# Kernel optimization log

Measured on AMD Instinct MI355X. Metric: run time of the kernel, lower is better.

## Reference

```python
import jax, jax.numpy as jnp
import numpy as np

EMB = 1024
HEADS = 16
HEAD_DIM = EMB // HEADS
DFF = 4 * EMB
EPS = 1e-5


def setup_inputs() -> dict:
    key = jax.random.key(0)
    ks = jax.random.split(key, 16)
    s = 0.02
    return {
        "x": jax.random.normal(ks[0], (4, 2048, EMB), dtype=jnp.float32),
        "Wq_w": jax.random.normal(ks[1], (EMB, EMB), jnp.float32) * s,
        "Wq_b": jnp.zeros((EMB,), jnp.float32),
        "Wk_w": jax.random.normal(ks[2], (EMB, EMB), jnp.float32) * s,
        "Wk_b": jnp.zeros((EMB,), jnp.float32),
        "Wv_w": jax.random.normal(ks[3], (EMB, EMB), jnp.float32) * s,
        "Wv_b": jnp.zeros((EMB,), jnp.float32),
        "Wo_w": jax.random.normal(ks[4], (EMB, EMB), jnp.float32) * s,
        "Wo_b": jnp.zeros((EMB,), jnp.float32),
        "l1_w": jax.random.normal(ks[5], (DFF, EMB), jnp.float32) * s,
        "l1_b": jnp.zeros((DFF,), jnp.float32),
        "l2_w": jax.random.normal(ks[6], (EMB, DFF), jnp.float32) * s,
        "l2_b": jnp.zeros((EMB,), jnp.float32),
        "n1_scale": jnp.ones((EMB,), jnp.float32),
        "n1_shift": jnp.zeros((EMB,), jnp.float32),
        "n2_scale": jnp.ones((EMB,), jnp.float32),
        "n2_shift": jnp.zeros((EMB,), jnp.float32),
    }


def _layernorm(x, scale, shift):
    # Faithful to the source: mean over last dim, but var over the WHOLE
    # tensor (torch.var with no dim), and divides by var (not std), eps added after.
    mean = jnp.mean(x, axis=-1, keepdims=True)
    var = jnp.var(x)  # scalar, correction=0
    x_norm = (x - mean) / var + EPS
    return x_norm * scale + shift


def _block_forward(x, Wq_w, Wq_b, Wk_w, Wk_b, Wv_w, Wv_b, Wo_w, Wo_b,
                   l1_w, l1_b, l2_w, l2_b, n1_scale, n1_shift, n2_scale, n2_shift):
    B, T, C = x.shape
    shortcut = x
    h = _layernorm(x, n1_scale, n1_shift)

    def proj(w, b):
        y = jnp.einsum('btc,oc->bto', h, w) + b
        return y.reshape(B, T, HEADS, HEAD_DIM).transpose(0, 2, 1, 3)  # bhtd

    q = proj(Wq_w, Wq_b)
    k = proj(Wk_w, Wk_b)
    v = proj(Wv_w, Wv_b)

    scores = jnp.einsum('bhtd,bhsd->bhts', q, k)
    causal = jnp.triu(jnp.ones((T, T), dtype=bool), 1)
    scores = jnp.where(causal, -jnp.inf, scores)
    weights = jax.nn.softmax(scores / jnp.sqrt(jnp.float32(HEAD_DIM)), axis=-1)
    ctx = jnp.einsum('bhts,bhsd->bhtd', weights, v)
    ctx = ctx.transpose(0, 2, 1, 3).reshape(B, T, C)
    attn_out = jnp.einsum('btc,oc->bto', ctx, Wo_w) + Wo_b

    x = attn_out + shortcut
    shortcut = x
    h = _layernorm(x, n2_scale, n2_shift)
    h = jnp.einsum('btc,fc->btf', h, l1_w) + l1_b
    h = jax.nn.gelu(h, approximate=False)
    h = jnp.einsum('btf,cf->btc', h, l2_w) + l2_b
    return h + shortcut


def reference(x, Wq_w, Wq_b, Wk_w, Wk_b, Wv_w, Wv_b, Wo_w, Wo_b,
              l1_w, l1_b, l2_w, l2_b, n1_scale, n1_shift, n2_scale, n2_shift):
    return _block_forward(x, Wq_w, Wq_b, Wk_w, Wk_b, Wv_w, Wv_b, Wo_w, Wo_b,
                          l1_w, l1_b, l2_w, l2_b, n1_scale, n1_shift, n2_scale, n2_shift)
```

## Files before the change

### kernel.cpp

```cpp
#include <hip/hip_runtime.h>
#include <cstdint>

#define EMB   1024
#define HEADS 16
#define HDIM  64
#define DFF   4096
#define TLEN  2048
#define BATCH 4
#define SEQB  8192
#define EPSLN 1e-5f

typedef __attribute__((ext_vector_type(8))) short bf16x8;
typedef __attribute__((ext_vector_type(4))) float f32x4;

#define MFMA16(a, b, c) __builtin_amdgcn_mfma_f32_16x16x32_bf16((a), (b), (c), 0, 0, 0)

__device__ __forceinline__ unsigned short f2bf(float f) {
  unsigned int u = __float_as_uint(f);
  u += 0x7fffu + ((u >> 16) & 1u);
  return (unsigned short)(u >> 16);
}

__device__ __forceinline__ float gelu_f(float x) {
  float x2 = x * x;
  float inner = x * (0.79788456f + 0.035677408f * x2);
  float t = exp2f(2.885390082f * inner);
  return x * t / (t + 1.0f);
}

__global__ __launch_bounds__(256) void cvt_bf16(const float* __restrict__ in,
                                                unsigned short* __restrict__ out, int n4) {
  int i = blockIdx.x * 256 + threadIdx.x;
  if (i >= n4) return;
  float4 v = ((const float4*)in)[i];
  ushort4 o;
  o.x = f2bf(v.x); o.y = f2bf(v.y); o.z = f2bf(v.z); o.w = f2bf(v.w);
  ((ushort4*)out)[i] = o;
}

__global__ __launch_bounds__(256) void pack3(const float* __restrict__ a,
                                             const float* __restrict__ b,
                                             const float* __restrict__ c,
                                             float* __restrict__ o) {
  int i = blockIdx.x * 256 + threadIdx.x;
  o[i] = i < 1024 ? a[i] : (i < 2048 ? b[i - 1024] : c[i - 2048]);
}

__global__ __launch_bounds__(256) void row_reduce(const float* __restrict__ X,
                                                  float* __restrict__ rs,
                                                  float* __restrict__ rq) {
  const int row = blockIdx.x;
  const int tid = threadIdx.x;
  float4 v = ((const float4*)(X + (long)row * EMB))[tid];
  float s = v.x + v.y + v.z + v.w;
  float q = v.x * v.x + v.y * v.y + v.z * v.z + v.w * v.w;
#pragma unroll
  for (int d = 1; d < 64; d <<= 1) { s += __shfl_xor(s, d); q += __shfl_xor(q, d); }
  __shared__ float ss[4], sq[4];
  const int wv = tid >> 6;
  if ((tid & 63) == 0) { ss[wv] = s; sq[wv] = q; }
  __syncthreads();
  if (tid == 0) {
    rs[row] = ss[0] + ss[1] + ss[2] + ss[3];
    rq[row] = sq[0] + sq[1] + sq[2] + sq[3];
  }
}

__global__ __launch_bounds__(256) void finalize_stats(const float* __restrict__ rs,
                                                      const float* __restrict__ rq,
                                                      float* __restrict__ stats) {
  const int tid = threadIdx.x;
  float s = 0.f, q = 0.f;
  for (int i = tid; i < SEQB; i += 256) { s += rs[i]; q += rq[i]; }
#pragma unroll
  for (int d = 1; d < 64; d <<= 1) { s += __shfl_xor(s, d); q += __shfl_xor(q, d); }
  __shared__ float ss[4], sq[4];
  const int wv = tid >> 6;
  if ((tid & 63) == 0) { ss[wv] = s; sq[wv] = q; }
  __syncthreads();
  if (tid == 0) {
    double n = (double)SEQB * (double)EMB;
    double mean = (double)(ss[0] + ss[1] + ss[2] + ss[3]) / n;
    double var = (double)(sq[0] + sq[1] + sq[2] + sq[3]) / n - mean * mean;
    stats[0] = (float)(1.0 / var);
  }
}

__global__ __launch_bounds__(256) void ln_apply(const float* __restrict__ X,
                                                const float* __restrict__ rs,
                                                const float* __restrict__ stats,
                                                const float* __restrict__ scale,
                                                const float* __restrict__ shift,
                                                unsigned short* __restrict__ H) {
  const long i = (long)blockIdx.x * 256 + threadIdx.x;
  const long idx = i * 4;
  const int row = (int)(idx >> 10);
  const int c = (int)(idx & 1023);
  const float mean = rs[row] * (1.0f / EMB);
  const float iv = stats[0];
  float4 x = ((const float4*)X)[i];
  float4 sc = *(const float4*)(scale + c);
  float4 sh = *(const float4*)(shift + c);
  ushort4 o;
  o.x = f2bf(((x.x - mean) * iv + EPSLN) * sc.x + sh.x);
  o.y = f2bf(((x.y - mean) * iv + EPSLN) * sc.y + sh.y);
  o.z = f2bf(((x.z - mean) * iv + EPSLN) * sc.z + sh.z);
  o.w = f2bf(((x.w - mean) * iv + EPSLN) * sc.w + sh.w);
  ((ushort4*)H)[i] = o;
}

template <int EPI>
__global__ __launch_bounds__(256) void gemm_bt(const unsigned short* __restrict__ A,
                                               const unsigned short* __restrict__ W,
                                               const float* __restrict__ bias,
                                               const float* __restrict__ resid,
                                               void* __restrict__ Cout,
                                               unsigned short* __restrict__ kout,
                                               unsigned short* __restrict__ vout,
                                               int M, int N, int K) {
  __shared__ unsigned short sA[128 * 64];
  __shared__ unsigned short sB[128 * 64];
  const int tid = threadIdx.x;
  const int lane = tid & 63;
  const int wave = tid >> 6;
  const int wm = (wave >> 1) * 64, wn = (wave & 1) * 64;
  const int col = lane & 15, quad = lane >> 4;
  const int cx = (col & 7) * 8;

  const int gx = (int)gridDim.x, gy = (int)gridDim.y;
  const int nwg = gx * gy;
  int bid = (int)blockIdx.y * gx + (int)blockIdx.x;
  if ((nwg & 7) == 0) bid = (bid & 7) * (nwg >> 3) + (bid >> 3);
  const int bx = bid % gx;
  const int by = bid / gx;
  const long bm = (long)by * 128, bn = (long)bx * 128;

  f32x4 acc[4][4];
#pragma unroll
  for (int i = 0; i < 4; ++i)
#pragma unroll
    for (int j = 0; j < 4; ++j) acc[i][j] = (f32x4){0.f, 0.f, 0.f, 0.f};

  const int r0 = tid >> 3;
  const int kg = (tid & 7) * 8;
  const int rx = (r0 & 7) * 8;
  const int kgx = kg ^ rx;

  for (int k0 = 0; k0 < K; k0 += 64) {
#pragma unroll
    for (int it = 0; it < 4; ++it) {
      const int r = it * 32 + r0;
      const unsigned short* ga = A + (bm + r) * K + k0 + kgx;
      const unsigned short* gb = W + (bn + r) * K + k0 + kgx;
      __builtin_amdgcn_global_load_lds((const __attribute__((address_space(1))) void*)ga,
                                       (__attribute__((address_space(3))) void*)&sA[r * 64 + kg],
                                       16, 0, 0);
      __builtin_amdgcn_global_load_lds((const __attribute__((address_space(1))) void*)gb,
                                       (__attribute__((address_space(3))) void*)&sB[r * 64 + kg],
                                       16, 0, 0);
    }
    __syncthreads();
#pragma unroll
    for (int ks = 0; ks < 2; ++ks) {
      const int off = (ks * 32 + quad * 8) ^ cx;
      bf16x8 af[4], bfr[4];
#pragma unroll
      for (int mt = 0; mt < 4; ++mt)
        af[mt] = *(const bf16x8*)&sA[(wm + mt * 16 + col) * 64 + off];
#pragma unroll
      for (int nt = 0; nt < 4; ++nt)
        bfr[nt] = *(const bf16x8*)&sB[(wn + nt * 16 + col) * 64 + off];
#pragma unroll
      for (int mt = 0; mt < 4; ++mt)
#pragma unroll
        for (int nt = 0; nt < 4; ++nt) acc[mt][nt] = MFMA16(af[mt], bfr[nt], acc[mt][nt]);
    }
    __syncthreads();
  }

#pragma unroll
  for (int mt = 0; mt < 4; ++mt) {
    const long row0 = bm + wm + mt * 16 + quad * 4;
#pragma unroll
    for (int nt = 0; nt < 4; ++nt) {
      const long c = bn + wn + nt * 16 + col;
      const float bv = bias[c];
      if (EPI == 4) {
        const int seg = (int)(bn >> 10);
        if (seg == 2) {
          ushort4 o;
#pragma unroll
          for (int r = 0; r < 4; ++r) o[r] = f2bf(acc[mt][nt][r] + bv);
          const long bidx = row0 >> 11;
          const long t0 = row0 & 2047;
          *(ushort4*)(vout + (((bidx * 1024 + (c & 1023)) << 11) + t0)) = o;
        } else {
          unsigned short* dst = seg == 0 ? (unsigned short*)Cout : kout;
#pragma unroll
          for (int r = 0; r < 4; ++r)
            dst[(row0 + r) * 1024 + (c & 1023)] = f2bf(acc[mt][nt][r] + bv);
        }
      } else {
#pragma unroll
        for (int r = 0; r < 4; ++r) {
          const long row = row0 + r;
          float v = acc[mt][nt][r] + bv;
          if (EPI == 0) {
            ((unsigned short*)Cout)[row * N + c] = f2bf(v);
          } else if (EPI == 1) {
            ((float*)Cout)[row * N + c] = v + resid[row * N + c];
          } else {
            ((unsigned short*)Cout)[row * N + c] = f2bf(gelu_f(v));
          }
        }
      }
    }
  }
}

#define PSTR 136
__global__ __launch_bounds__(512, 4) void attn10(const unsigned short* __restrict__ Qb,
                                                 const unsigned short* __restrict__ Kb,
                                                 const unsigned short* __restrict__ vT,
                                                 unsigned short* __restrict__ Ctx) {
  __shared__ unsigned short sK[128 * 64];
  __shared__ unsigned short sV[64 * 128];
  __shared__ unsigned short sP[8][16 * PSTR];
  const int bh = blockIdx.x;
  const int pair = blockIdx.y;
  const int b = bh >> 4, h = bh & 15;
  const int tid = threadIdx.x, lane = tid & 63, w = tid >> 6;
  const int col = lane & 15, quad = lane >> 4;
  const int cx = (col & 7) * 8;
  const long bbase = (long)b * TLEN;
  const long hoff = (long)h * HDIM;
  const unsigned short* vbase = vT + (((long)b * 16 + h) * HDIM << 11);
  const float sc2 = 0.125f * 1.44269504088896340736f;

  const int krow = tid >> 3;
  const int kcol = ((tid & 7) * 8) ^ ((krow & 7) * 8);
  const int vrow = tid >> 4;
  const int vcol = ((tid & 15) * 8) ^ ((vrow & 7) * 8);

  for (int phase = 0; phase < 2; ++phase) {
    const int qt = phase == 0 ? (15 - pair) : pair;

    bf16x8 qf[2];
    {
      const long t = (long)qt * 128 + w * 16 + col;
      const unsigned short* qp = Qb + (bbase + t) * EMB + hoff;
#pragma unroll
      for (int ks = 0; ks < 2; ++ks) qf[ks] = *(const bf16x8*)(qp + ks * 32 + quad * 8);
    }

    float li[4] = {0.f, 0.f, 0.f, 0.f};
    f32x4 o[4];
#pragma unroll
    for (int dt = 0; dt < 4; ++dt) o[dt] = (f32x4){0.f, 0.f, 0.f, 0.f};

    for (int kv = 0; kv <= qt; ++kv) {
      __syncthreads();
#pragma unroll
      for (int it = 0; it < 2; ++it) {
        const unsigned short* gk = Kb + (bbase + (long)kv * 128 + it * 64 + krow) * EMB + hoff + kcol;
        __builtin_amdgcn_global_load_lds((const __attribute__((address_space(1))) void*)gk,
                                         (__attribute__((address_space(3))) void*)&sK[it * 4096 + tid * 8],
                                         16, 0, 0);
        const unsigned short* gv = vbase + ((long)(it * 32 + vrow) << 11) + kv * 128 + vcol;
        __builtin_amdgcn_global_load_lds((const __attribute__((address_space(1))) void*)gv,
                                         (__attribute__((address_space(3))) void*)&sV[it * 4096 + tid * 8],
                                         16, 0, 0);
      }
      __syncthreads();

      f32x4 sa[8];
#pragma unroll
      for (int nt = 0; nt < 8; ++nt) sa[nt] = (f32x4){0.f, 0.f, 0.f, 0.f};
#pragma unroll
      for (int ks = 0; ks < 2; ++ks) {
        const int off = (ks * 32 + quad * 8) ^ cx;
#pragma unroll
        for (int nt = 0; nt < 8; ++nt) {
          bf16x8 kf = *(const bf16x8*)&sK[(nt * 16 + col) * 64 + off];
          sa[nt] = MFMA16(qf[ks], kf, sa[nt]);
        }
      }

      if (kv == qt) {
#pragma unroll
        for (int nt = 0; nt < 8; ++nt)
#pragma unroll
          for (int r = 0; r < 4; ++r) {
            const int trel = w * 16 + quad * 4 + r;
            const int srel = nt * 16 + col;
            if (srel > trel) sa[nt][r] = -INFINITY;
          }
      }

#pragma unroll
      for (int nt = 0; nt < 8; ++nt)
#pragma unroll
        for (int r = 0; r < 4; ++r) {
          const float p = exp2f(sa[nt][r] * sc2);
          li[r] += p;
          sP[w][(quad * 4 + r) * PSTR + nt * 16 + col] = f2bf(p);
        }

#pragma unroll
      for (int ks = 0; ks < 4; ++ks) {
        bf16x8 pa = *(const bf16x8*)&sP[w][col * PSTR + ks * 32 + quad * 8];
        const int voff = (ks * 32 + quad * 8) ^ cx;
#pragma unroll
        for (int dt = 0; dt < 4; ++dt) {
          bf16x8 vf = *(const bf16x8*)&sV[(dt * 16 + col) * 128 + voff];
          o[dt] = MFMA16(pa, vf, o[dt]);
        }
      }
    }

#pragma unroll
    for (int d = 1; d < 16; d <<= 1)
#pragma unroll
      for (int r = 0; r < 4; ++r) li[r] += __shfl_xor(li[r], d);

#pragma unroll
    for (int r = 0; r < 4; ++r) {
      const float inv = 1.0f / li[r];
#pragma unroll
      for (int dt = 0; dt < 4; ++dt)
        sP[w][(quad * 4 + r) * 72 + dt * 16 + col] = f2bf(o[dt][r] * inv);
    }
#pragma unroll
    for (int p = 0; p < 2; ++p) {
      const int rr = (lane >> 3) + p * 8;
      bf16x8 vrow = *(const bf16x8*)&sP[w][rr * 72 + (lane & 7) * 8];
      const long t = (long)qt * 128 + w * 16 + rr;
      *(bf16x8*)(Ctx + (bbase + t) * EMB + hoff + (lane & 7) * 8) = vrow;
    }
  }
}

extern "C" void kernel_launch(void* const* d_in, const int* in_sizes, int n_in,
                              void* d_out, int out_size, void* d_ws, size_t ws_size,
                              hipStream_t stream) {
  const float* x    = (const float*)d_in[0];
  const float* Wq_w = (const float*)d_in[1];
  const float* Wq_b = (const float*)d_in[2];
  const float* Wk_w = (const float*)d_in[3];
  const float* Wk_b = (const float*)d_in[4];
  const float* Wv_w = (const float*)d_in[5];
  const float* Wv_b = (const float*)d_in[6];
  const float* Wo_w = (const float*)d_in[7];
  const float* Wo_b = (const float*)d_in[8];
  const float* l1_w = (const float*)d_in[9];
  const float* l1_b = (const float*)d_in[10];
  const float* l2_w = (const float*)d_in[11];
  const float* l2_b = (const float*)d_in[12];
  const float* n1s  = (const float*)d_in[13];
  const float* n1h  = (const float*)d_in[14];
  const float* n2s  = (const float*)d_in[15];
  const float* n2h  = (const float*)d_in[16];

  char* ws = (char*)d_ws;
  const size_t MB = (size_t)1 << 20;
  unsigned short* wqkv = (unsigned short*)(ws + 0 * MB);
  unsigned short* wo = (unsigned short*)(ws + 6 * MB);
  unsigned short* l1 = (unsigned short*)(ws + 8 * MB);
  unsigned short* l2 = (unsigned short*)(ws + 16 * MB);
  unsigned short* hb = (unsigned short*)(ws + 24 * MB);
  unsigned short* qb = (unsigned short*)(ws + 40 * MB);
  unsigned short* kb = (unsigned short*)(ws + 56 * MB);
  unsigned short* vb = (unsigned short*)(ws + 72 * MB);
  unsigned short* cb = (unsigned short*)(ws + 88 * MB);
  unsigned short* gb = qb;
  float* x2 = (float*)(ws + 104 * MB);
  float* rs = (float*)(ws + 136 * MB);
  float* rq = (float*)(ws + 136 * MB + 64 * 1024);
  float* st = (float*)(ws + 136 * MB + 128 * 1024);
  float* bqkv = (float*)(ws + 136 * MB + 192 * 1024);

  cvt_bf16<<<1024, 256, 0, stream>>>(Wq_w, wqkv, EMB * EMB / 4);
  cvt_bf16<<<1024, 256, 0, stream>>>(Wk_w, wqkv + 1024 * 1024, EMB * EMB / 4);
  cvt_bf16<<<1024, 256, 0, stream>>>(Wv_w, wqkv + 2048 * 1024, EMB * EMB / 4);
  cvt_bf16<<<1024, 256, 0, stream>>>(Wo_w, wo, EMB * EMB / 4);
  cvt_bf16<<<4096, 256, 0, stream>>>(l1_w, l1, DFF * EMB / 4);
  cvt_bf16<<<4096, 256, 0, stream>>>(l2_w, l2, EMB * DFF / 4);
  pack3<<<12, 256, 0, stream>>>(Wq_b, Wk_b, Wv_b, bqkv);

  row_reduce<<<SEQB, 256, 0, stream>>>(x, rs, rq);
  finalize_stats<<<1, 256, 0, stream>>>(rs, rq, st);
  ln_apply<<<SEQB, 256, 0, stream>>>(x, rs, st, n1s, n1h, hb);

  dim3 g1(EMB / 128, SEQB / 128);
  gemm_bt<4><<<dim3(3 * EMB / 128, SEQB / 128), 256, 0, stream>>>(
      hb, wqkv, bqkv, nullptr, qb, kb, vb, SEQB, 3 * EMB, EMB);

  attn10<<<dim3(BATCH * HEADS, 8), 512, 0, stream>>>(qb, kb, vb, cb);

  gemm_bt<1><<<g1, 256, 0, stream>>>(cb, wo, Wo_b, x, (void*)x2, nullptr, nullptr, SEQB, EMB, EMB);

  row_reduce<<<SEQB, 256, 0, stream>>>(x2, rs, rq);
  finalize_stats<<<1, 256, 0, stream>>>(rs, rq, st);
  ln_apply<<<SEQB, 256, 0, stream>>>(x2, rs, st, n2s, n2h, hb);

  gemm_bt<2><<<dim3(DFF / 128, SEQB / 128), 256, 0, stream>>>(hb, l1, l1_b, nullptr, gb, nullptr, nullptr, SEQB, DFF, EMB);
  gemm_bt<1><<<g1, 256, 0, stream>>>(gb, l2, l2_b, x2, d_out, nullptr, nullptr, SEQB, EMB, DFF);
}
```

Before: 540.6 us.

## Fuse prep kernels and compute LN2 row stats in out-proj GEMM epilogue

Merges the six weight-conversion launches, the bias packing, the first row-reduction and the zeroing of new stat buffers into one large prep kernel. Adds a GEMM epilogue variant for the attention output projection that adds the residual and accumulates per-row sum and sum-of-squares via shuffles and atomics. This removes the separate row_reduce pass over x2. In exchange it adds atomic traffic and float-ordering nondeterminism in the row statistics.

Measured after the change: 540.7 us. Within noise of the previous version (+0.0%).

```diff
diff --git a/kernel.cpp b/kernel.cpp
--- a/kernel.cpp
+++ b/kernel.cpp
@@ -28,41 +28,55 @@
   return x * t / (t + 1.0f);
 }
 
-__global__ __launch_bounds__(256) void cvt_bf16(const float* __restrict__ in,
-                                                unsigned short* __restrict__ out, int n4) {
-  int i = blockIdx.x * 256 + threadIdx.x;
-  if (i >= n4) return;
-  float4 v = ((const float4*)in)[i];
-  ushort4 o;
-  o.x = f2bf(v.x); o.y = f2bf(v.y); o.z = f2bf(v.z); o.w = f2bf(v.w);
-  ((ushort4*)out)[i] = o;
-}
-
-__global__ __launch_bounds__(256) void pack3(const float* __restrict__ a,
-                                             const float* __restrict__ b,
-                                             const float* __restrict__ c,
-                                             float* __restrict__ o) {
-  int i = blockIdx.x * 256 + threadIdx.x;
-  o[i] = i < 1024 ? a[i] : (i < 2048 ? b[i - 1024] : c[i - 2048]);
-}
-
-__global__ __launch_bounds__(256) void row_reduce(const float* __restrict__ X,
-                                                  float* __restrict__ rs,
-                                                  float* __restrict__ rq) {
-  const int row = blockIdx.x;
+__global__ __launch_bounds__(256) void prep(const float* __restrict__ wq, const float* __restrict__ wk,
+                                            const float* __restrict__ wv, const float* __restrict__ wom,
+                                            const float* __restrict__ l1w, const float* __restrict__ l2w,
+                                            unsigned short* __restrict__ wqkv, unsigned short* __restrict__ wo,
+                                            unsigned short* __restrict__ l1, unsigned short* __restrict__ l2,
+                                            const float* __restrict__ bq, const float* __restrict__ bk,
+                                            const float* __restrict__ bv, float* __restrict__ bqkv,
+                                            const float* __restrict__ X, float* __restrict__ rs,
+                                            float* __restrict__ rq, float* __restrict__ rs2,
+                                            float* __restrict__ rq2) {
+  __shared__ float ss[4], sq[4];
+  const int bid = blockIdx.x;
   const int tid = threadIdx.x;
-  float4 v = ((const float4*)(X + (long)row * EMB))[tid];
-  float s = v.x + v.y + v.z + v.w;
-  float q = v.x * v.x + v.y * v.y + v.z * v.z + v.w * v.w;
-#pragma unroll
-  for (int d = 1; d < 64; d <<= 1) { s += __shfl_xor(s, d); q += __shfl_xor(q, d); }
-  __shared__ float ss[4], sq[4];
-  const int wv = tid >> 6;
-  if ((tid & 63) == 0) { ss[wv] = s; sq[wv] = q; }
-  __syncthreads();
-  if (tid == 0) {
-    rs[row] = ss[0] + ss[1] + ss[2] + ss[3];
-    rq[row] = sq[0] + sq[1] + sq[2] + sq[3];
+  if (bid < 12288) {
+    const float* src;
+    unsigned short* dst;
+    int off;
+    if (bid < 1024)      { src = wq;  dst = wqkv;               off = bid; }
+    else if (bid < 2048) { src = wk;  dst = wqkv + (1 << 20);   off = bid - 1024; }
+    else if (bid < 3072) { src = wv;  dst = wqkv + (2 << 20);   off = bid - 2048; }
+    else if (bid < 4096) { src = wom; dst = wo;                 off = bid - 3072; }
+    else if (bid < 8192) { src = l1w; dst = l1;                 off = bid - 4096; }
+    else                 { src = l2w; dst = l2;                 off = bid - 8192; }
+    const int i = off * 256 + tid;
+    float4 v = ((const float4*)src)[i];
+    ushort4 o;
+    o.x = f2bf(v.x); o.y = f2bf(v.y); o.z = f2bf(v.z); o.w = f2bf(v.w);
+    ((ushort4*)dst)[i] = o;
+  } else if (bid < 20480) {
+    const int row = bid - 12288;
+    float4 v = ((const float4*)(X + (long)row * EMB))[tid];
+    float s = v.x + v.y + v.z + v.w;
+    float q = v.x * v.x + v.y * v.y + v.z * v.z + v.w * v.w;
+#pragma unroll
+    for (int d = 1; d < 64; d <<= 1) { s += __shfl_xor(s, d); q += __shfl_xor(q, d); }
+    const int wv_ = tid >> 6;
+    if ((tid & 63) == 0) { ss[wv_] = s; sq[wv_] = q; }
+    __syncthreads();
+    if (tid == 0) {
+      rs[row] = ss[0] + ss[1] + ss[2] + ss[3];
+      rq[row] = sq[0] + sq[1] + sq[2] + sq[3];
+    }
+  } else if (bid < 20492) {
+    const int i = (bid - 20480) * 256 + tid;
+    bqkv[i] = i < 1024 ? bq[i] : (i < 2048 ? bk[i - 1024] : bv[i - 2048]);
+  } else {
+    const int i = (bid - 20492) * 256 + tid;
+    if (i < 2048) ((float4*)rs2)[i] = (float4){0.f, 0.f, 0.f, 0.f};
+    else          ((float4*)rq2)[i - 2048] = (float4){0.f, 0.f, 0.f, 0.f};
   }
 }
 
@@ -181,36 +195,67 @@
 #pragma unroll
   for (int mt = 0; mt < 4; ++mt) {
     const long row0 = bm + wm + mt * 16 + quad * 4;
-#pragma unroll
-    for (int nt = 0; nt < 4; ++nt) {
-      const long c = bn + wn + nt * 16 + col;
-      const float bv = bias[c];
-      if (EPI == 4) {
-        const int seg = (int)(bn >> 10);
-        if (seg == 2) {
-          ushort4 o;
-#pragma unroll
-          for (int r = 0; r < 4; ++r) o[r] = f2bf(acc[mt][nt][r] + bv);
-          const long bidx = row0 >> 11;
-          const long t0 = row0 & 2047;
-          *(ushort4*)(vout + (((bidx * 1024 + (c & 1023)) << 11) + t0)) = o;
-        } else {
-          unsigned short* dst = seg == 0 ? (unsigned short*)Cout : kout;
-#pragma unroll
-          for (int r = 0; r < 4; ++r)
-            dst[(row0 + r) * 1024 + (c & 1023)] = f2bf(acc[mt][nt][r] + bv);
-        }
-      } else {
+    if (EPI == 3) {
+      float s4[4] = {0.f, 0.f, 0.f, 0.f}, q4[4] = {0.f, 0.f, 0.f, 0.f};
+#pragma unroll
+      for (int nt = 0; nt < 4; ++nt) {
+        const long c = bn + wn + nt * 16 + col;
+        const float bv = bias[c];
 #pragma unroll
         for (int r = 0; r < 4; ++r) {
           const long row = row0 + r;
-          float v = acc[mt][nt][r] + bv;
-          if (EPI == 0) {
-            ((unsigned short*)Cout)[row * N + c] = f2bf(v);
-          } else if (EPI == 1) {
-            ((float*)Cout)[row * N + c] = v + resid[row * N + c];
+          const float v = acc[mt][nt][r] + bv + resid[row * N + c];
+          ((float*)Cout)[row * N + c] = v;
+          s4[r] += v;
+          q4[r] += v * v;
+        }
+      }
+#pragma unroll
+      for (int r = 0; r < 4; ++r)
+#pragma unroll
+        for (int d = 1; d < 16; d <<= 1) {
+          s4[r] += __shfl_xor(s4[r], d);
+          q4[r] += __shfl_xor(q4[r], d);
+        }
+      if (col == 0) {
+#pragma unroll
+        for (int r = 0; r < 4; ++r) {
+          atomicAdd((float*)kout + row0 + r, s4[r]);
+          atomicAdd((float*)vout + row0 + r, q4[r]);
+        }
+      }
+    } else {
+#pragma unroll
+      for (int nt = 0; nt < 4; ++nt) {
+        const long c = bn + wn + nt * 16 + col;
+        const float bv = bias[c];
+        if (EPI == 4) {
+          const int seg = (int)(bn >> 10);
+          if (seg == 2) {
+            ushort4 o;
+#pragma unroll
+            for (int r = 0; r < 4; ++r) o[r] = f2bf(acc[mt][nt][r] + bv);
+            const long bidx = row0 >> 11;
+            const long t0 = row0 & 2047;
+            *(ushort4*)(vout + (((bidx * 1024 + (c & 1023)) << 11) + t0)) = o;
           } else {
-            ((unsigned short*)Cout)[row * N + c] = f2bf(gelu_f(v));
+            unsigned short* dst = seg == 0 ? (unsigned short*)Cout : kout;
+#pragma unroll
+            for (int r = 0; r < 4; ++r)
+              dst[(row0 + r) * 1024 + (c & 1023)] = f2bf(acc[mt][nt][r] + bv);
+          }
+        } else {
+#pragma unroll
+          for (int r = 0; r < 4; ++r) {
+            const long row = row0 + r;
+            float v = acc[mt][nt][r] + bv;
+            if (EPI == 0) {
+              ((unsigned short*)Cout)[row * N + c] = f2bf(v);
+            } else if (EPI == 1) {
+              ((float*)Cout)[row * N + c] = v + resid[row * N + c];
+            } else {
+              ((unsigned short*)Cout)[row * N + c] = f2bf(gelu_f(v));
+            }
           }
         }
       }
@@ -378,16 +423,12 @@
   float* rq = (float*)(ws + 136 * MB + 64 * 1024);
   float* st = (float*)(ws + 136 * MB + 128 * 1024);
   float* bqkv = (float*)(ws + 136 * MB + 192 * 1024);
-
-  cvt_bf16<<<1024, 256, 0, stream>>>(Wq_w, wqkv, EMB * EMB / 4);
-  cvt_bf16<<<1024, 256, 0, stream>>>(Wk_w, wqkv + 1024 * 1024, EMB * EMB / 4);
-  cvt_bf16<<<1024, 256, 0, stream>>>(Wv_w, wqkv + 2048 * 1024, EMB * EMB / 4);
-  cvt_bf16<<<1024, 256, 0, stream>>>(Wo_w, wo, EMB * EMB / 4);
-  cvt_bf16<<<4096, 256, 0, stream>>>(l1_w, l1, DFF * EMB / 4);
-  cvt_bf16<<<4096, 256, 0, stream>>>(l2_w, l2, EMB * DFF / 4);
-  pack3<<<12, 256, 0, stream>>>(Wq_b, Wk_b, Wv_b, bqkv);
-
-  row_reduce<<<SEQB, 256, 0, stream>>>(x, rs, rq);
+  float* rs2 = (float*)(ws + 136 * MB + 256 * 1024);
+  float* rq2 = (float*)(ws + 136 * MB + 320 * 1024);
+
+  prep<<<20508, 256, 0, stream>>>(Wq_w, Wk_w, Wv_w, Wo_w, l1_w, l2_w, wqkv, wo, l1, l2,
+                                  Wq_b, Wk_b, Wv_b, bqkv, x, rs, rq, rs2, rq2);
+
   finalize_stats<<<1, 256, 0, stream>>>(rs, rq, st);
   ln_apply<<<SEQB, 256, 0, stream>>>(x, rs, st, n1s, n1h, hb);
 
@@ -397,11 +438,11 @@
 
   attn10<<<dim3(BATCH * HEADS, 8), 512, 0, stream>>>(qb, kb, vb, cb);
 
-  gemm_bt<1><<<g1, 256, 0, stream>>>(cb, wo, Wo_b, x, (void*)x2, nullptr, nullptr, SEQB, EMB, EMB);
-
-  row_reduce<<<SEQB, 256, 0, stream>>>(x2, rs, rq);
-  finalize_stats<<<1, 256, 0, stream>>>(rs, rq, st);
-  ln_apply<<<SEQB, 256, 0, stream>>>(x2, rs, st, n2s, n2h, hb);
+  gemm_bt<3><<<g1, 256, 0, stream>>>(cb, wo, Wo_b, x, (void*)x2,
+                                     (unsigned short*)rs2, (unsigned short*)rq2, SEQB, EMB, EMB);
+
+  finalize_stats<<<1, 256, 0, stream>>>(rs2, rq2, st);
+  ln_apply<<<SEQB, 256, 0, stream>>>(x2, rs2, st, n2s, n2h, hb);
 
   gemm_bt<2><<<dim3(DFF / 128, SEQB / 128), 256, 0, stream>>>(hb, l1, l1_b, nullptr, gb, nullptr, nullptr, SEQB, DFF, EMB);
   gemm_bt<1><<<g1, 256, 0, stream>>>(gb, l2, l2_b, x2, d_out, nullptr, nullptr, SEQB, EMB, DFF);
```
